# Kernel optimization log

Measured on AMD Instinct MI355X. Metric: run time of the kernel, lower is better.

## Reference

```python
import jax, jax.numpy as jnp
import numpy as np

D = 384      # d_model
DM = 256     # memory feature dim
DF = 1536    # dim_feedforward
EPS = 1e-5


def _layer_norm(x, g, b):
    m = jnp.mean(x, axis=-1, keepdims=True)
    v = jnp.mean(jnp.square(x - m), axis=-1, keepdims=True)
    return (x - m) * jax.lax.rsqrt(v + EPS) * g + b


def setup_inputs() -> dict:
    key = jax.random.key(0)
    ks = jax.random.split(key, 24)
    B, T, T1, Tc = 8, 2048, 2048, 2048
    s = 0.02
    inp = {
        "tgt": jax.random.normal(ks[0], (B, T, D), jnp.float32),
        "memory": jax.random.normal(ks[1], (B, T1, DM), jnp.float32),
        "a1": jnp.float32(0.5),
        "score_c": jax.random.normal(ks[2], (B, 1, Tc, T1), jnp.float32) * 0.1,
        "out_c": jax.random.normal(ks[3], (B, Tc, D), jnp.float32),
        # attention projections
        "Wq": jax.random.normal(ks[4], (D, D), jnp.float32) * s,
        "bq": jnp.zeros((D,), jnp.float32),
        "Wk": jax.random.normal(ks[5], (DM, D), jnp.float32) * s,
        "bk": jnp.zeros((D,), jnp.float32),
        "Wv": jax.random.normal(ks[6], (DM, D), jnp.float32) * s,
        "bv": jnp.zeros((D,), jnp.float32),
        "Wu": jax.random.normal(ks[7], (D, D), jnp.float32) * s,  # unknown
        "bu": jnp.zeros((D,), jnp.float32),
        "Wn": jax.random.normal(ks[8], (D, D), jnp.float32) * s,  # known
        "bn": jnp.zeros((D,), jnp.float32),
        # FFN
        "W1": jax.random.normal(ks[9], (D, DF), jnp.float32) * s,
        "b1": jnp.zeros((DF,), jnp.float32),
        "W2": jax.random.normal(ks[10], (DF, D), jnp.float32) * s,
        "b2": jnp.zeros((D,), jnp.float32),
        # LayerNorms
        "g1": jnp.ones((D,), jnp.float32),
        "be1": jnp.zeros((D,), jnp.float32),
        "g2": jnp.ones((D,), jnp.float32),
        "be2": jnp.zeros((D,), jnp.float32),
    }
    return inp


def reference(tgt, memory, a1, score_c, out_c,
              Wq, bq, Wk, bk, Wv, bv, Wu, bu, Wn, bn,
              W1, b1, W2, b2, g1, be1, g2, be2):
    # --- En_De_Attention (n_head = 1; dropout p=0 / eval mode -> identity) ---
    scale = 1.0 / jnp.sqrt(jnp.float32(D))
    q = tgt @ Wq + bq                  # [B,T,D]
    k = memory @ Wk + bk               # [B,T1,D]
    v = memory @ Wv + bv               # [B,T1,D]
    att = jnp.einsum('btd,bsd->bts', q, k) * scale            # [B,T,T1]

    unknow = tgt @ Wu + bu             # [B,T,D]
    know = out_c @ Wn + bn             # [B,Tc,D]
    score1 = jnp.einsum('btd,bcd->btc', unknow, know) * scale  # [B,T,Tc]
    mixed = jnp.einsum('btc,bcs->bts', score1, score_c[:, 0])  # [B,T,T1]

    # tt = a1 in (0,1]: blended-score branch of the original module
    score = a1 * jax.nn.softmax(mixed, axis=-1) \
          + (1.0 - a1) * jax.nn.softmax(att, axis=-1)          # [B,T,T1]
    z = jnp.einsum('bts,bsd->btd', score, v)                   # [B,T,D]

    # --- residual + norm1 ---
    x = _layer_norm(tgt + z, g1, be1)
    # --- FFN (relu) + residual + norm2 (dropout eval -> identity) ---
    ff = jax.nn.relu(x @ W1 + b1) @ W2 + b2
    out = _layer_norm(x + ff, g2, be2)
    # score2 returned with head dim, matching torch shape [B,1,T,T1]
    return out, score[:, None]
```

## Files before the change

kernel.cpp:

```cpp
#include <hip/hip_runtime.h>
#include <stdint.h>

typedef __attribute__((ext_vector_type(8))) short bf16x8;
typedef __attribute__((ext_vector_type(4))) float f32x4;

__device__ __forceinline__ short f2bf(float f) {
    union { float f; unsigned u; } v; v.f = f;
    unsigned r = v.u + 0x7fffu + ((v.u >> 16) & 1u);
    return (short)(r >> 16);
}
__device__ __forceinline__ float bf2f(short s) {
    union { unsigned u; float f; } v;
    v.u = ((unsigned)(unsigned short)s) << 16;
    return v.f;
}

__device__ __forceinline__ void gld16(const void* g, void* l) {
    auto gp = reinterpret_cast<const __attribute__((address_space(1))) unsigned int*>(
        reinterpret_cast<uintptr_t>(g));
    auto lp = reinterpret_cast<__attribute__((address_space(3))) unsigned int*>(
        reinterpret_cast<uintptr_t>(l));
    __builtin_amdgcn_global_load_lds(gp, lp, 16, 0, 0);
}

template<int OUTBF, int BIASMODE , int DORELU>
__global__ __launch_bounds__(256, 2) void gemmWide(
    const short* __restrict__ Ag, const short* __restrict__ Bg,
    void* __restrict__ Cg, const float* __restrict__ bias,
    int K, int lda, int ldb, int ldc,
    long long sA, long long sB, long long sC,
    long long dA, long long dB, long long dC, float scale)
{
    __shared__ short lds[3 * 12288];
    const int t = threadIdx.x;
    const int lane = t & 63;
    const int wave = t >> 6;
    const int wm = wave >> 1, wn = wave & 1;

    const int gx = gridDim.x, gy = gridDim.y;
    const int nwg = gx * gy * gridDim.z;
    int id = blockIdx.x + gx * (blockIdx.y + gy * blockIdx.z);
    id = (id & 7) * (nwg >> 3) + (id >> 3);
    const int bx = id % gx;
    const int by = (id / gx) % gy;
    const int bz = id / (gx * gy);
    const int zlo = bz & 7, zhi = bz >> 3;

    const long long row0 = (long long)by * 128;
    const long long col0 = (long long)bx * 256;
    const int NT = K >> 5;

    const int gk = ((t & 3) ^ ((t >> 2) & 3) ^ ((t >> 4) & 3)) * 8;
    const short* Asrc = Ag + zlo * sA + zhi * dA + (row0 + (t >> 2)) * (long long)lda + gk;
    const short* Bsrc = Bg + zlo * sB + zhi * dB + (col0 + (t >> 2)) * (long long)ldb + gk;

    const int frow = lane & 15;
    const int fcol = ((lane >> 4) ^ (frow & 3) ^ ((frow >> 2) & 3)) * 8;

    f32x4 acc[4][8] = {};

#define STG(BUF, KC) do { \
        gld16(Asrc + (KC), &lds[(BUF) * 12288 + t * 8]); \
        gld16(Asrc + (KC) + 64LL * lda, &lds[(BUF) * 12288 + 2048 + t * 8]); \
        gld16(Bsrc + (KC), &lds[(BUF) * 12288 + 4096 + t * 8]); \
        gld16(Bsrc + (KC) + 64LL * ldb, &lds[(BUF) * 12288 + 6144 + t * 8]); \
        gld16(Bsrc + (KC) + 128LL * ldb, &lds[(BUF) * 12288 + 8192 + t * 8]); \
        gld16(Bsrc + (KC) + 192LL * ldb, &lds[(BUF) * 12288 + 10240 + t * 8]); } while (0)

    STG(0, 0);
    STG(1, 32);
    asm volatile("s_waitcnt vmcnt(6)\ns_barrier" ::: "memory");

    for (int kt = 0; kt < NT; ++kt) {
        const int rb = (kt % 3) * 12288;
        bf16x8 av[4], bv[8];
#pragma unroll
        for (int m = 0; m < 4; ++m)
            av[m] = *(const bf16x8*)&lds[rb + (wm * 64 + m * 16 + frow) * 32 + fcol];
#pragma unroll
        for (int n = 0; n < 8; ++n)
            bv[n] = *(const bf16x8*)&lds[rb + 4096 + (wn * 128 + n * 16 + frow) * 32 + fcol];
        if (kt + 2 < NT) STG((kt + 2) % 3, (long long)(kt + 2) * 32);
        __builtin_amdgcn_s_setprio(1);
#pragma unroll
        for (int m = 0; m < 4; ++m)
#pragma unroll
            for (int n = 0; n < 8; ++n)
                acc[m][n] = __builtin_amdgcn_mfma_f32_16x16x32_bf16(av[m], bv[n], acc[m][n], 0, 0, 0);
        __builtin_amdgcn_s_setprio(0);
        if (kt + 1 < NT) {
            if (kt + 2 < NT) asm volatile("s_waitcnt vmcnt(6)\ns_barrier" ::: "memory");
            else             asm volatile("s_waitcnt vmcnt(0)\ns_barrier" ::: "memory");
        }
    }
#undef STG

    const int crow = (lane >> 4) * 4;
    const int ccol = lane & 15;
    const long long cz = zlo * sC + zhi * dC;
#pragma unroll
    for (int m = 0; m < 4; ++m)
#pragma unroll
        for (int n = 0; n < 8; ++n)
#pragma unroll
            for (int i = 0; i < 4; ++i) {
                long long r = row0 + wm * 64 + m * 16 + crow + i;
                long long c = col0 + wn * 128 + n * 16 + ccol;
                float v = acc[m][n][i] * scale;
                if (BIASMODE == 1) v += bias[c];
                if (DORELU) v = fmaxf(v, 0.0f);
                long long idx = cz + r * (long long)ldc + c;
                if (OUTBF) ((short*)Cg)[idx] = f2bf(v);
                else ((float*)Cg)[idx] = v;
            }
}

template<int OUTBF, int BIASMODE , int DORELU>
__global__ __launch_bounds__(256, 3) void gemm128r(
    const short* __restrict__ Ag, const short* __restrict__ Bg,
    void* __restrict__ Cg, const float* __restrict__ bias,
    int K, int lda, int ldb, int ldc,
    long long sA, long long sB, long long sC,
    long long dA, long long dB, long long dC, float scale)
{
    __shared__ short lds[3 * 8192];
    const int t = threadIdx.x;
    const int lane = t & 63;
    const int wave = t >> 6;
    const int wm = wave >> 1, wn = wave & 1;

    const int gx = gridDim.x, gy = gridDim.y;
    const int nwg = gx * gy * gridDim.z;
    int id = blockIdx.x + gx * (blockIdx.y + gy * blockIdx.z);
    id = (id & 7) * (nwg >> 3) + (id >> 3);
    const int bx = id % gx;
    const int by = (id / gx) % gy;
    const int bz = id / (gx * gy);
    const int zlo = bz & 7, zhi = bz >> 3;

    const long long row0 = (long long)by * 128;
    const long long col0 = (long long)bx * 128;
    const int NT = K >> 5;

    const int gk = ((t & 3) ^ ((t >> 2) & 3) ^ ((t >> 4) & 3)) * 8;
    const short* Asrc = Ag + zlo * sA + zhi * dA + (row0 + (t >> 2)) * (long long)lda + gk;
    const short* Bsrc = Bg + zlo * sB + zhi * dB + (col0 + (t >> 2)) * (long long)ldb + gk;

    const int frow = lane & 15;
    const int fcol = ((lane >> 4) ^ (frow & 3) ^ ((frow >> 2) & 3)) * 8;

    f32x4 acc[4][4] = {};

#define STG(BUF, KC) do { \
        gld16(Asrc + (KC), &lds[(BUF) * 8192 + t * 8]); \
        gld16(Asrc + (KC) + 64LL * lda, &lds[(BUF) * 8192 + 2048 + t * 8]); \
        gld16(Bsrc + (KC), &lds[(BUF) * 8192 + 4096 + t * 8]); \
        gld16(Bsrc + (KC) + 64LL * ldb, &lds[(BUF) * 8192 + 6144 + t * 8]); } while (0)

    STG(0, 0);
    STG(1, 32);
    asm volatile("s_waitcnt vmcnt(4)\ns_barrier" ::: "memory");

    for (int kt = 0; kt < NT; ++kt) {
        const int rb = (kt % 3) * 8192;
        bf16x8 av[4], bv[4];
#pragma unroll
        for (int m = 0; m < 4; ++m)
            av[m] = *(const bf16x8*)&lds[rb + (wm * 64 + m * 16 + frow) * 32 + fcol];
#pragma unroll
        for (int n = 0; n < 4; ++n)
            bv[n] = *(const bf16x8*)&lds[rb + 4096 + (wn * 64 + n * 16 + frow) * 32 + fcol];
        if (kt + 2 < NT) STG((kt + 2) % 3, (long long)(kt + 2) * 32);
        __builtin_amdgcn_s_setprio(1);
#pragma unroll
        for (int m = 0; m < 4; ++m)
#pragma unroll
            for (int n = 0; n < 4; ++n)
                acc[m][n] = __builtin_amdgcn_mfma_f32_16x16x32_bf16(av[m], bv[n], acc[m][n], 0, 0, 0);
        __builtin_amdgcn_s_setprio(0);
        if (kt + 1 < NT) {
            if (kt + 2 < NT) asm volatile("s_waitcnt vmcnt(4)\ns_barrier" ::: "memory");
            else             asm volatile("s_waitcnt vmcnt(0)\ns_barrier" ::: "memory");
        }
    }
#undef STG

    const int crow = (lane >> 4) * 4;
    const int ccol = lane & 15;
    const long long cz = zlo * sC + zhi * dC;
#pragma unroll
    for (int m = 0; m < 4; ++m)
#pragma unroll
        for (int n = 0; n < 4; ++n)
#pragma unroll
            for (int i = 0; i < 4; ++i) {
                long long r = row0 + wm * 64 + m * 16 + crow + i;
                long long c = col0 + wn * 64 + n * 16 + ccol;
                float v = acc[m][n][i] * scale;
                if (BIASMODE == 1) v += bias[c];
                if (BIASMODE == 2) v += bias[r];
                if (DORELU) v = fmaxf(v, 0.0f);
                long long idx = cz + r * (long long)ldc + c;
                if (OUTBF) ((short*)Cg)[idx] = f2bf(v);
                else ((float*)Cg)[idx] = v;
            }
}

#define RD_A(RB, M, KS) (*(const bf16x8*)&lds[(RB) + (wm * 64 + (M) * 16 + frow) * 64 + \
        ((((KS) << 2) | fq) ^ (frow & 7)) * 8])
#define RD_B(RB, Nn, KS) (*(const bf16x8*)&lds[(RB) + 8192 + (wn * 64 + (Nn) * 16 + frow) * 64 + \
        ((((KS) << 2) | fq) ^ (frow & 7)) * 8])

__global__ __launch_bounds__(256, 2) void gemm128pz(
    const short* __restrict__ A1, const short* __restrict__ B1, short* __restrict__ C1,
    const float* __restrict__ bias1, int K1, int lda1, int ldb1, int ldc1,
    long long sB1, long long sC1,
    const short* __restrict__ A2, const short* __restrict__ B2, short* __restrict__ C2,
    const float* __restrict__ bias2, int K2, int lda2, int ldb2, int ldc2,
    long long sB2, long long sC2)
{
    __shared__ short lds[2 * 16384];
    const int t = threadIdx.x;
    const int lane = t & 63;
    const int wave = t >> 6;
    const int wm = wave >> 1, wn = wave & 1;

    const int gx = gridDim.x, gy = gridDim.y;
    const int nwg = gx * gy * gridDim.z;
    int id = blockIdx.x + gx * (blockIdx.y + gy * blockIdx.z);
    id = (id & 7) * (nwg >> 3) + (id >> 3);
    const int bx = id % gx;
    const int by = (id / gx) % gy;
    const int bz = id / (gx * gy);

    const bool sel = bz >= 8;
    const int zz = bz & 7;
    const short* Ag = sel ? A2 : A1;
    const short* Bg = sel ? B2 : B1;
    short* Cg = sel ? C2 : C1;
    const float* bias = sel ? bias2 : bias1;
    const int K = sel ? K2 : K1;
    const int lda = sel ? lda2 : lda1;
    const int ldb = sel ? ldb2 : ldb1;
    const int ldc = sel ? ldc2 : ldc1;
    const long long sB = sel ? sB2 : sB1;
    const long long sC = sel ? sC2 : sC1;

    const long long row0 = (long long)by * 128;
    const long long col0 = (long long)bx * 128;
    const int NT = K >> 6;

    const int srow = t >> 3;
    const int gk = ((t & 7) ^ (srow & 7)) * 8;
    const short* Asrc = Ag + (row0 + srow) * (long long)lda + gk;
    const short* Bsrc = Bg + (long long)zz * sB + (col0 + srow) * (long long)ldb + gk;

    const int frow = lane & 15;
    const int fq = lane >> 4;

    f32x4 acc[4][4] = {};

#define STAGE_A(WB, KC) do { _Pragma("unroll") \
        for (int r = 0; r < 4; ++r) \
            gld16(Asrc + (KC) + (long long)r * 32 * lda, &lds[(WB) + t * 8 + r * 2048]); } while (0)
#define STAGE_B(WB, KC) do { _Pragma("unroll") \
        for (int r = 0; r < 4; ++r) \
            gld16(Bsrc + (KC) + (long long)r * 32 * ldb, &lds[(WB) + 8192 + t * 8 + r * 2048]); } while (0)

    STAGE_A(0, 0);
    STAGE_B(0, 0);
    asm volatile("s_waitcnt vmcnt(0)\ns_barrier" ::: "memory");

    for (int kt = 0; kt < NT; ++kt) {
        const int rb = (kt & 1) << 14;
        const int wb = ((kt + 1) & 1) << 14;
        const bool st = (kt + 1) < NT;
        const long long kc = (long long)(kt + 1) << 6;

        bf16x8 av[4], bv[4];

#pragma unroll
        for (int m = 0; m < 4; ++m) av[m] = RD_A(rb, m, 0);
#pragma unroll
        for (int n = 0; n < 4; ++n) bv[n] = RD_B(rb, n, 0);
        if (st) STAGE_A(wb, kc);
        asm volatile("s_barrier" ::: "memory");
        __builtin_amdgcn_s_setprio(1);
#pragma unroll
        for (int m = 0; m < 4; ++m)
#pragma unroll
            for (int n = 0; n < 4; ++n)
                acc[m][n] = __builtin_amdgcn_mfma_f32_16x16x32_bf16(av[m], bv[n], acc[m][n], 0, 0, 0);
        __builtin_amdgcn_s_setprio(0);
        asm volatile("s_barrier" ::: "memory");

#pragma unroll
        for (int m = 0; m < 4; ++m) av[m] = RD_A(rb, m, 1);
#pragma unroll
        for (int n = 0; n < 4; ++n) bv[n] = RD_B(rb, n, 1);
        if (st) STAGE_B(wb, kc);
        asm volatile("s_barrier" ::: "memory");
        __builtin_amdgcn_s_setprio(1);
#pragma unroll
        for (int m = 0; m < 4; ++m)
#pragma unroll
            for (int n = 0; n < 4; ++n)
                acc[m][n] = __builtin_amdgcn_mfma_f32_16x16x32_bf16(av[m], bv[n], acc[m][n], 0, 0, 0);
        __builtin_amdgcn_s_setprio(0);
        if (st) asm volatile("s_waitcnt vmcnt(0)\ns_barrier" ::: "memory");
        else    asm volatile("s_barrier" ::: "memory");
    }
#undef STAGE_A
#undef STAGE_B

    const int crow = (lane >> 4) * 4;
    const int ccol = lane & 15;
    const long long cz = (long long)zz * sC;
#pragma unroll
    for (int m = 0; m < 4; ++m)
#pragma unroll
        for (int n = 0; n < 4; ++n)
#pragma unroll
            for (int i = 0; i < 4; ++i) {
                long long r = row0 + wm * 64 + m * 16 + crow + i;
                long long c = col0 + wn * 64 + n * 16 + ccol;
                float v = acc[m][n][i] + bias[r];
                Cg[cz + r * (long long)ldc + c] = f2bf(v);
            }
}
#undef RD_A
#undef RD_B

__global__ __launch_bounds__(256) void cast_all(
    const float* __restrict__ tgt, const float* __restrict__ mem, const float* __restrict__ outc,
    const float* __restrict__ bq, const float* __restrict__ bu,
    short* __restrict__ tgtb, short* __restrict__ memb, short* __restrict__ outcb,
    float* __restrict__ qubias)
{
    const long long R1 = 1572864;
    const long long R2 = R1 + 1048576;
    const long long R3 = R2 + 1572864;
    const long long R4 = R3 + 192;
    long long i = (long long)blockIdx.x * 256 + threadIdx.x;
    const float* in; short* out; long long j;
    if (i < R1) { in = tgt; out = tgtb; j = i; }
    else if (i < R2) { in = mem; out = memb; j = i - R1; }
    else if (i < R3) { in = outc; out = outcb; j = i - R2; }
    else if (i < R4) {
        j = i - R3;
        ((float4*)qubias)[j] = (j < 96) ? ((const float4*)bq)[j] : ((const float4*)bu)[j - 96];
        return;
    } else return;
    float4 v = ((const float4*)in)[j];
    short4 o;
    o.x = f2bf(v.x); o.y = f2bf(v.y); o.z = f2bf(v.z); o.w = f2bf(v.w);
    ((short4*)out)[j] = o;
}

__global__ __launch_bounds__(256) void transpose_all(
    const float* __restrict__ Wq, const float* __restrict__ Wk, const float* __restrict__ Wv,
    const float* __restrict__ Wu, const float* __restrict__ Wn,
    const float* __restrict__ W1, const float* __restrict__ W2,
    short* __restrict__ WquT, short* __restrict__ WkT, short* __restrict__ WvT,
    short* __restrict__ WnT, short* __restrict__ W1T, short* __restrict__ W2T)
{
    __shared__ float tile[64][65];
    int b = blockIdx.x;
    const float* in; short* out; int R, C, local;
    if (b < 36)       { in = Wq; out = WquT;          R = 384;  C = 384;  local = b; }
    else if (b < 60)  { in = Wk; out = WkT;           R = 256;  C = 384;  local = b - 36; }
    else if (b < 84)  { in = Wv; out = WvT;           R = 256;  C = 384;  local = b - 60; }
    else if (b < 120) { in = Wu; out = WquT + 147456; R = 384;  C = 384;  local = b - 84; }
    else if (b < 156) { in = Wn; out = WnT;           R = 384;  C = 384;  local = b - 120; }
    else if (b < 300) { in = W1; out = W1T;           R = 384;  C = 1536; local = b - 156; }
    else              { in = W2; out = W2T;           R = 1536; C = 384;  local = b - 300; }
    const int nbx = C >> 6;
    const int r0 = (local / nbx) * 64, c0 = (local % nbx) * 64;
    const int lr = threadIdx.x >> 6, lc = threadIdx.x & 63;
#pragma unroll
    for (int i = 0; i < 16; ++i) {
        int r = lr * 16 + i;
        tile[r][lc] = in[(long long)(r0 + r) * C + c0 + lc];
    }
    __syncthreads();
#pragma unroll
    for (int i = 0; i < 16; ++i) {
        int r = lr * 16 + i;
        out[(long long)(c0 + r) * R + r0 + lc] = f2bf(tile[lc][r]);
    }
}

__global__ __launch_bounds__(256) void transpose_cast(
    const float* __restrict__ in, short* __restrict__ out,
    int R, int C, long long sIn, long long sOut)
{
    __shared__ float tile[64][65];
    const long long zi = (long long)blockIdx.z * sIn;
    const long long zo = (long long)blockIdx.z * sOut;
    const int r0 = blockIdx.y * 64, c0 = blockIdx.x * 64;
    const int lr = threadIdx.x >> 6, lc = threadIdx.x & 63;
#pragma unroll
    for (int i = 0; i < 16; ++i) {
        int r = lr * 16 + i;
        tile[r][lc] = in[zi + (long long)(r0 + r) * C + c0 + lc];
    }
    __syncthreads();
#pragma unroll
    for (int i = 0; i < 16; ++i) {
        int r = lr * 16 + i;
        out[zo + (long long)(c0 + r) * R + r0 + lc] = f2bf(tile[lc][r]);
    }
}

__global__ __launch_bounds__(256) void softmax_blend(
    const short* __restrict__ attb, const short* __restrict__ mixb,
    const float* __restrict__ a1p,
    float* __restrict__ outF, short* __restrict__ outB)
{
    const int S = 2048;
    const long long row = blockIdx.x;
    const short* ar = attb + row * S;
    const short* mr = mixb + row * S;
    const int t = threadIdx.x;
    const int wave = t >> 6;

    bf16x8 a8 = *(const bf16x8*)&ar[t * 8];
    bf16x8 m8 = *(const bf16x8*)&mr[t * 8];
    float av[8], mv[8];
#pragma unroll
    for (int i = 0; i < 8; ++i) { av[i] = bf2f(a8[i]); mv[i] = bf2f(m8[i]); }

    float amax = av[0], mmax = mv[0];
#pragma unroll
    for (int i = 1; i < 8; ++i) { amax = fmaxf(amax, av[i]); mmax = fmaxf(mmax, mv[i]); }
#pragma unroll
    for (int o = 32; o; o >>= 1) {
        amax = fmaxf(amax, __shfl_xor(amax, o));
        mmax = fmaxf(mmax, __shfl_xor(mmax, o));
    }
    __shared__ float red[2][4];
    if ((t & 63) == 0) { red[0][wave] = amax; red[1][wave] = mmax; }
    __syncthreads();
    amax = fmaxf(fmaxf(red[0][0], red[0][1]), fmaxf(red[0][2], red[0][3]));
    mmax = fmaxf(fmaxf(red[1][0], red[1][1]), fmaxf(red[1][2], red[1][3]));

    float asum = 0.f, msum = 0.f;
#pragma unroll
    for (int i = 0; i < 8; ++i) {
        av[i] = __expf(av[i] - amax); asum += av[i];
        mv[i] = __expf(mv[i] - mmax); msum += mv[i];
    }
#pragma unroll
    for (int o = 32; o; o >>= 1) {
        asum += __shfl_xor(asum, o);
        msum += __shfl_xor(msum, o);
    }
    __shared__ float red2[2][4];
    if ((t & 63) == 0) { red2[0][wave] = asum; red2[1][wave] = msum; }
    __syncthreads();
    asum = red2[0][0] + red2[0][1] + red2[0][2] + red2[0][3];
    msum = red2[1][0] + red2[1][1] + red2[1][2] + red2[1][3];

    const float a1 = a1p[0];
    const float wm = a1 / msum;
    const float wa = (1.0f - a1) / asum;

    float o0[8];
    bf16x8 ob;
#pragma unroll
    for (int i = 0; i < 8; ++i) {
        float s = wm * mv[i] + wa * av[i];
        o0[i] = s;
        ob[i] = f2bf(s);
    }
    float4 f0, f1;
    f0.x = o0[0]; f0.y = o0[1]; f0.z = o0[2]; f0.w = o0[3];
    f1.x = o0[4]; f1.y = o0[5]; f1.z = o0[6]; f1.w = o0[7];
    *(float4*)&outF[row * S + t * 8] = f0;
    *(float4*)&outF[row * S + t * 8 + 4] = f1;
    *(bf16x8*)&outB[row * S + t * 8] = ob;
}

template<int WRITE_BF, int TWO_Y>
__global__ __launch_bounds__(256) void ln_kernel(
    const float* __restrict__ X, const float* __restrict__ Yr,
    const float* __restrict__ Y2,
    const float* __restrict__ g, const float* __restrict__ be,
    float* __restrict__ outF, short* __restrict__ outB)
{
    const int Dm = 384;
    const int wave = threadIdx.x >> 6, lane = threadIdx.x & 63;
    const long long row = (long long)blockIdx.x * 4 + wave;
    const float* x = X + row * Dm;
    const float* y = Yr + row * Dm;
    const float* y2 = TWO_Y ? (Y2 + row * Dm) : nullptr;
    float h[6];
    float s = 0.f, s2 = 0.f;
#pragma unroll
    for (int j = 0; j < 6; ++j) {
        int c = j * 64 + lane;
        h[j] = x[c] + y[c];
        if (TWO_Y) h[j] += y2[c];
        s += h[j]; s2 += h[j] * h[j];
    }
#pragma unroll
    for (int o = 32; o; o >>= 1) { s += __shfl_xor(s, o); s2 += __shfl_xor(s2, o); }
    const float mean = s * (1.0f / 384.0f);
    const float var = s2 * (1.0f / 384.0f) - mean * mean;
    const float rstd = rsqrtf(var + 1e-5f);
#pragma unroll
    for (int j = 0; j < 6; ++j) {
        int c = j * 64 + lane;
        float v = (h[j] - mean) * rstd * g[c] + be[c];
        outF[row * Dm + c] = v;
        if (WRITE_BF) outB[row * Dm + c] = f2bf(v);
    }
}

extern "C" void kernel_launch(void* const* d_in, const int* in_sizes, int n_in,
                              void* d_out, int out_size, void* d_ws, size_t ws_size,
                              hipStream_t stream) {
    const float* tgt     = (const float*)d_in[0];
    const float* memory  = (const float*)d_in[1];
    const float* a1      = (const float*)d_in[2];
    const float* score_c = (const float*)d_in[3];
    const float* out_c   = (const float*)d_in[4];
    const float* Wq = (const float*)d_in[5];  const float* bq = (const float*)d_in[6];
    const float* Wk = (const float*)d_in[7];  const float* bk = (const float*)d_in[8];
    const float* Wv = (const float*)d_in[9];  const float* bv = (const float*)d_in[10];
    const float* Wu = (const float*)d_in[11]; const float* bu = (const float*)d_in[12];
    const float* Wn = (const float*)d_in[13]; const float* bn = (const float*)d_in[14];
    const float* W1 = (const float*)d_in[15]; const float* b1 = (const float*)d_in[16];
    const float* W2 = (const float*)d_in[17]; const float* b2 = (const float*)d_in[18];
    const float* g1 = (const float*)d_in[19]; const float* be1 = (const float*)d_in[20];
    const float* g2 = (const float*)d_in[21]; const float* be2 = (const float*)d_in[22];

    const long long BT = 16384;
    const long long S2 = 2048LL * 2048;
    const long long PB = 2048LL * 384;
    char* ws = (char*)d_ws;
    size_t off = 0;
    auto A_ = [&](size_t b) { size_t r = off; off += (b + 255) & ~(size_t)255; return r; };

    const size_t oTgtB  = A_(BT * 384 * 2);
    const size_t oMemB  = A_(BT * 256 * 2);
    const size_t oOutcB = A_(BT * 384 * 2);
    const size_t oWquT  = A_(768 * 384 * 2);
    const size_t oWnT   = A_(384 * 384 * 2);
    const size_t oWkT   = A_(384 * 256 * 2);
    const size_t oWvT   = A_(384 * 256 * 2);
    const size_t oW1T   = A_(1536 * 384 * 2);
    const size_t oW2T   = A_(384 * 1536 * 2);
    const size_t oQUb   = A_(768 * 4);
    const size_t oQU    = A_(16 * PB * 2);
    const size_t oKP    = A_(16 * PB * 2);
    const size_t oVT    = A_(8LL * 384 * 2048 * 2);
    const size_t oJ     = A_(8 * S2 * 2);
    const size_t oKr    = A_(8 * S2 * 2);
    const size_t oAM    = A_(16 * S2 * 2);
    const size_t oX     = A_(BT * 384 * 4);
    const size_t oXB    = A_(BT * 384 * 2);

    short* tgt_bf  = (short*)(ws + oTgtB);
    short* mem_bf  = (short*)(ws + oMemB);
    short* outc_bf = (short*)(ws + oOutcB);
    short* WquT = (short*)(ws + oWquT);
    short* WnT  = (short*)(ws + oWnT);
    short* WkT  = (short*)(ws + oWkT);
    short* WvT  = (short*)(ws + oWvT);
    short* W1T  = (short*)(ws + oW1T);
    short* W2T  = (short*)(ws + oW2T);
    float* qu_bias = (float*)(ws + oQUb);
    short* qu_bf  = (short*)(ws + oQU);
    short* k_bf   = (short*)(ws + oKP);
    short* Pt_bf  = k_bf + 8 * PB;
    short* vT_bf  = (short*)(ws + oVT);
    short* score_bf = (short*)(ws + oJ);
    short* scoreCt  = (short*)(ws + oKr);
    float* z0_f     = (float*)(ws + oKr);
    float* z1_f     = z0_f + 6291456;
    short* knoT_bf  = (short*)(ws + oAM);
    short* att_bf   = (short*)(ws + oAM);
    short* mix_bf   = att_bf + 8 * S2;
    short* h_bf     = (short*)(ws + oAM);
    float* ff_f     = (float*)(ws + oAM + 8 * S2 * 2);
    float* x_f  = (float*)(ws + oX);
    short* x_bf = (short*)(ws + oXB);

    float* outMain = (float*)d_out;
    float* outScore = (float*)d_out + 6291456;

    const float SC = 0.05103103630798288f;
    dim3 blk(256);

    cast_all<<<16385, blk, 0, stream>>>(tgt, memory, out_c, bq, bu,
                                        tgt_bf, mem_bf, outc_bf, qu_bias);
    transpose_all<<<444, blk, 0, stream>>>(Wq, Wk, Wv, Wu, Wn, W1, W2,
                                           WquT, WkT, WvT, WnT, W1T, W2T);
    transpose_cast<<<dim3(32, 32, 8), blk, 0, stream>>>(score_c, scoreCt, 2048, 2048, S2, S2);

    gemmWide<1, 1, 0><<<dim3(3, 128, 1), blk, 0, stream>>>(
        tgt_bf, WquT, qu_bf, qu_bias, 384, 384, 384, 768, 0, 0, 0, 0, 0, 0, 1.0f);
    gemm128r<1, 1, 0><<<dim3(3, 128, 1), blk, 0, stream>>>(
        mem_bf, WkT, k_bf, bk, 256, 256, 256, 384, 0, 0, 0, 0, 0, 0, 1.0f);
    gemm128pz<<<dim3(16, 3, 16), blk, 0, stream>>>(
        WvT, mem_bf, vT_bf, bv, 256, 256, 256, 2048, 2048LL * 256, PB,
        WnT, outc_bf, knoT_bf, bn, 384, 384, 384, 2048, PB, PB);
    gemm128r<1, 0, 0><<<dim3(3, 16, 8), blk, 0, stream>>>(
        scoreCt, knoT_bf, Pt_bf, nullptr, 2048, 2048, 2048, 384,
        S2, PB, PB, 0, 0, 0, 1.0f);
    gemmWide<1, 0, 0><<<dim3(8, 16, 16), blk, 0, stream>>>(
        qu_bf, k_bf, att_bf, nullptr, 384, 768, 384, 2048,
        2048LL * 768, PB, S2, 384, 8 * PB, 8 * S2, SC);
    softmax_blend<<<16384, blk, 0, stream>>>(att_bf, mix_bf, a1, outScore, score_bf);
    gemm128r<0, 0, 0><<<dim3(3, 16, 16), blk, 0, stream>>>(
        score_bf, vT_bf, z0_f, nullptr, 1024, 2048, 2048, 384,
        S2, PB, PB, 1024, 1024, 6291456, 1.0f);
    ln_kernel<1, 1><<<4096, blk, 0, stream>>>(tgt, z0_f, z1_f, g1, be1, x_f, x_bf);
    gemmWide<1, 1, 1><<<dim3(6, 128, 1), blk, 0, stream>>>(
        x_bf, W1T, h_bf, b1, 384, 384, 384, 1536, 0, 0, 0, 0, 0, 0, 1.0f);
    gemm128r<0, 1, 0><<<dim3(3, 128, 1), blk, 0, stream>>>(
        h_bf, W2T, ff_f, b2, 1536, 1536, 1536, 384, 0, 0, 0, 0, 0, 0, 1.0f);
    ln_kernel<0, 0><<<4096, blk, 0, stream>>>(x_f, ff_f, nullptr, g2, be2, outMain, nullptr);
}
```

Before: 446.9 us.

## Fuse prologue kernels, merge Q/K projections, drop fp32 LN1 output

Combines the cast, weight-transpose and score_c transpose kernels into one launch. Merges the QU and K projection GEMMs into a new 3-stage pipelined kernel with a block-id swizzle. LN1 now writes only bf16, and LN2 reads that bf16 tensor as its residual, which removes an fp32 write and read at some cost in residual precision. The FFN up-projection switches to the gemm128r tile kernel.

Result: faster. 430.4 us (-3.7%).

```diff
diff --git a/kernel.cpp b/kernel.cpp
--- a/kernel.cpp
+++ b/kernel.cpp
@@ -206,6 +206,100 @@
             }
 }
 
+__global__ __launch_bounds__(256, 3) void gemm128rr(
+    const short* __restrict__ A1, const short* __restrict__ B1,
+    short* __restrict__ C1, const float* __restrict__ bias1,
+    int K1, int lda1, int ldb1, int ldc1,
+    const short* __restrict__ A2, const short* __restrict__ B2,
+    short* __restrict__ C2, const float* __restrict__ bias2,
+    int K2, int lda2, int ldb2, int ldc2)
+{
+    __shared__ short lds[3 * 8192];
+    const int t = threadIdx.x;
+    const int lane = t & 63;
+    const int wave = t >> 6;
+    const int wm = wave >> 1, wn = wave & 1;
+
+    const int gx = gridDim.x, gy = gridDim.y;
+    const int nwg = gx * gy;
+    int id = blockIdx.x + gx * blockIdx.y;
+    id = (id & 7) * (nwg >> 3) + (id >> 3);
+    const int bx = id % gx;
+    const int by = id / gx;
+
+    const bool sel = bx >= 6;
+    const int bxx = sel ? bx - 6 : bx;
+    const short* Ag = sel ? A2 : A1;
+    const short* Bg = sel ? B2 : B1;
+    short* Cg = sel ? C2 : C1;
+    const float* bias = sel ? bias2 : bias1;
+    const int K = sel ? K2 : K1;
+    const int lda = sel ? lda2 : lda1;
+    const int ldb = sel ? ldb2 : ldb1;
+    const int ldc = sel ? ldc2 : ldc1;
+
+    const long long row0 = (long long)by * 128;
+    const long long col0 = (long long)bxx * 128;
+    const int NT = K >> 5;
+
+    const int gk = ((t & 3) ^ ((t >> 2) & 3) ^ ((t >> 4) & 3)) * 8;
+    const short* Asrc = Ag + (row0 + (t >> 2)) * (long long)lda + gk;
+    const short* Bsrc = Bg + (col0 + (t >> 2)) * (long long)ldb + gk;
+
+    const int frow = lane & 15;
+    const int fcol = ((lane >> 4) ^ (frow & 3) ^ ((frow >> 2) & 3)) * 8;
+
+    f32x4 acc[4][4] = {};
+
+#define STG(BUF, KC) do { \
+        gld16(Asrc + (KC), &lds[(BUF) * 8192 + t * 8]); \
+        gld16(Asrc + (KC) + 64LL * lda, &lds[(BUF) * 8192 + 2048 + t * 8]); \
+        gld16(Bsrc + (KC), &lds[(BUF) * 8192 + 4096 + t * 8]); \
+        gld16(Bsrc + (KC) + 64LL * ldb, &lds[(BUF) * 8192 + 6144 + t * 8]); } while (0)
+
+    STG(0, 0);
+    STG(1, 32);
+    asm volatile("s_waitcnt vmcnt(4)\ns_barrier" ::: "memory");
+
+    for (int kt = 0; kt < NT; ++kt) {
+        const int rb = (kt % 3) * 8192;
+        bf16x8 av[4], bv[4];
+#pragma unroll
+        for (int m = 0; m < 4; ++m)
+            av[m] = *(const bf16x8*)&lds[rb + (wm * 64 + m * 16 + frow) * 32 + fcol];
+#pragma unroll
+        for (int n = 0; n < 4; ++n)
+            bv[n] = *(const bf16x8*)&lds[rb + 4096 + (wn * 64 + n * 16 + frow) * 32 + fcol];
+        if (kt + 2 < NT) STG((kt + 2) % 3, (long long)(kt + 2) * 32);
+        __builtin_amdgcn_s_setprio(1);
+#pragma unroll
+        for (int m = 0; m < 4; ++m)
+#pragma unroll
+            for (int n = 0; n < 4; ++n)
+                acc[m][n] = __builtin_amdgcn_mfma_f32_16x16x32_bf16(av[m], bv[n], acc[m][n], 0, 0, 0);
+        __builtin_amdgcn_s_setprio(0);
+        if (kt + 1 < NT) {
+            if (kt + 2 < NT) asm volatile("s_waitcnt vmcnt(4)\ns_barrier" ::: "memory");
+            else             asm volatile("s_waitcnt vmcnt(0)\ns_barrier" ::: "memory");
+        }
+    }
+#undef STG
+
+    const int crow = (lane >> 4) * 4;
+    const int ccol = lane & 15;
+#pragma unroll
+    for (int m = 0; m < 4; ++m)
+#pragma unroll
+        for (int n = 0; n < 4; ++n)
+#pragma unroll
+            for (int i = 0; i < 4; ++i) {
+                long long r = row0 + wm * 64 + m * 16 + crow + i;
+                long long c = col0 + wn * 64 + n * 16 + ccol;
+                float v = acc[m][n][i] + bias[c];
+                Cg[r * (long long)ldc + c] = f2bf(v);
+            }
+}
+
 #define RD_A(RB, M, KS) (*(const bf16x8*)&lds[(RB) + (wm * 64 + (M) * 16 + frow) * 64 + \
         ((((KS) << 2) | fq) ^ (frow & 7)) * 8])
 #define RD_B(RB, Nn, KS) (*(const bf16x8*)&lds[(RB) + 8192 + (wn * 64 + (Nn) * 16 + frow) * 64 + \
@@ -331,84 +425,90 @@
 #undef RD_A
 #undef RD_B
 
-__global__ __launch_bounds__(256) void cast_all(
+__global__ __launch_bounds__(256) void prologue(
     const float* __restrict__ tgt, const float* __restrict__ mem, const float* __restrict__ outc,
     const float* __restrict__ bq, const float* __restrict__ bu,
     short* __restrict__ tgtb, short* __restrict__ memb, short* __restrict__ outcb,
-    float* __restrict__ qubias)
-{
-    const long long R1 = 1572864;
-    const long long R2 = R1 + 1048576;
-    const long long R3 = R2 + 1572864;
-    const long long R4 = R3 + 192;
-    long long i = (long long)blockIdx.x * 256 + threadIdx.x;
-    const float* in; short* out; long long j;
-    if (i < R1) { in = tgt; out = tgtb; j = i; }
-    else if (i < R2) { in = mem; out = memb; j = i - R1; }
-    else if (i < R3) { in = outc; out = outcb; j = i - R2; }
-    else if (i < R4) {
-        j = i - R3;
-        ((float4*)qubias)[j] = (j < 96) ? ((const float4*)bq)[j] : ((const float4*)bu)[j - 96];
-        return;
-    } else return;
-    float4 v = ((const float4*)in)[j];
-    short4 o;
-    o.x = f2bf(v.x); o.y = f2bf(v.y); o.z = f2bf(v.z); o.w = f2bf(v.w);
-    ((short4*)out)[j] = o;
-}
-
-__global__ __launch_bounds__(256) void transpose_all(
+    float* __restrict__ qubias,
     const float* __restrict__ Wq, const float* __restrict__ Wk, const float* __restrict__ Wv,
     const float* __restrict__ Wu, const float* __restrict__ Wn,
     const float* __restrict__ W1, const float* __restrict__ W2,
     short* __restrict__ WquT, short* __restrict__ WkT, short* __restrict__ WvT,
-    short* __restrict__ WnT, short* __restrict__ W1T, short* __restrict__ W2T)
+    short* __restrict__ WnT, short* __restrict__ W1T, short* __restrict__ W2T,
+    const float* __restrict__ score_c, short* __restrict__ scoreCt)
 {
     __shared__ float tile[64][65];
-    int b = blockIdx.x;
-    const float* in; short* out; int R, C, local;
-    if (b < 36)       { in = Wq; out = WquT;          R = 384;  C = 384;  local = b; }
-    else if (b < 60)  { in = Wk; out = WkT;           R = 256;  C = 384;  local = b - 36; }
-    else if (b < 84)  { in = Wv; out = WvT;           R = 256;  C = 384;  local = b - 60; }
-    else if (b < 120) { in = Wu; out = WquT + 147456; R = 384;  C = 384;  local = b - 84; }
-    else if (b < 156) { in = Wn; out = WnT;           R = 384;  C = 384;  local = b - 120; }
-    else if (b < 300) { in = W1; out = W1T;           R = 384;  C = 1536; local = b - 156; }
-    else              { in = W2; out = W2T;           R = 1536; C = 384;  local = b - 300; }
-    const int nbx = C >> 6;
-    const int r0 = (local / nbx) * 64, c0 = (local % nbx) * 64;
+    const int blk = blockIdx.x;
+
+    if (blk < 16385) {
+        const long long R1 = 1572864;
+        const long long R2 = R1 + 1048576;
+        const long long R3 = R2 + 1572864;
+        const long long R4 = R3 + 192;
+        long long i = (long long)blk * 256 + threadIdx.x;
+        const float* in; short* out; long long j;
+        if (i < R1) { in = tgt; out = tgtb; j = i; }
+        else if (i < R2) { in = mem; out = memb; j = i - R1; }
+        else if (i < R3) { in = outc; out = outcb; j = i - R2; }
+        else if (i < R4) {
+            j = i - R3;
+            ((float4*)qubias)[j] = (j < 96) ? ((const float4*)bq)[j] : ((const float4*)bu)[j - 96];
+            return;
+        } else return;
+        float4 v = ((const float4*)in)[j];
+        short4 o;
+        o.x = f2bf(v.x); o.y = f2bf(v.y); o.z = f2bf(v.z); o.w = f2bf(v.w);
+        ((short4*)out)[j] = o;
+        return;
+    }
+
     const int lr = threadIdx.x >> 6, lc = threadIdx.x & 63;
-#pragma unroll
-    for (int i = 0; i < 16; ++i) {
-        int r = lr * 16 + i;
-        tile[r][lc] = in[(long long)(r0 + r) * C + c0 + lc];
-    }
-    __syncthreads();
-#pragma unroll
-    for (int i = 0; i < 16; ++i) {
-        int r = lr * 16 + i;
-        out[(long long)(c0 + r) * R + r0 + lc] = f2bf(tile[lc][r]);
-    }
-}
-
-__global__ __launch_bounds__(256) void transpose_cast(
-    const float* __restrict__ in, short* __restrict__ out,
-    int R, int C, long long sIn, long long sOut)
-{
-    __shared__ float tile[64][65];
-    const long long zi = (long long)blockIdx.z * sIn;
-    const long long zo = (long long)blockIdx.z * sOut;
-    const int r0 = blockIdx.y * 64, c0 = blockIdx.x * 64;
-    const int lr = threadIdx.x >> 6, lc = threadIdx.x & 63;
-#pragma unroll
-    for (int i = 0; i < 16; ++i) {
-        int r = lr * 16 + i;
-        tile[r][lc] = in[zi + (long long)(r0 + r) * C + c0 + lc];
-    }
-    __syncthreads();
-#pragma unroll
-    for (int i = 0; i < 16; ++i) {
-        int r = lr * 16 + i;
-        out[zo + (long long)(c0 + r) * R + r0 + lc] = f2bf(tile[lc][r]);
+
+    if (blk < 16829) {
+        int b = blk - 16385;
+        const float* in; short* out; int R, C, local;
+        if (b < 36)       { in = Wq; out = WquT;          R = 384;  C = 384;  local = b; }
+        else if (b < 60)  { in = Wk; out = WkT;           R = 256;  C = 384;  local = b - 36; }
+        else if (b < 84)  { in = Wv; out = WvT;           R = 256;  C = 384;  local = b - 60; }
+        else if (b < 120) { in = Wu; out = WquT + 147456; R = 384;  C = 384;  local = b - 84; }
+        else if (b < 156) { in = Wn; out = WnT;           R = 384;  C = 384;  local = b - 120; }
+        else if (b < 300) { in = W1; out = W1T;           R = 384;  C = 1536; local = b - 156; }
+        else              { in = W2; out = W2T;           R = 1536; C = 384;  local = b - 300; }
+        const int nbx = C >> 6;
+        const int r0 = (local / nbx) * 64, c0 = (local % nbx) * 64;
+#pragma unroll
+        for (int i = 0; i < 16; ++i) {
+            int r = lr * 16 + i;
+            tile[r][lc] = in[(long long)(r0 + r) * C + c0 + lc];
+        }
+        __syncthreads();
+#pragma unroll
+        for (int i = 0; i < 16; ++i) {
+            int r = lr * 16 + i;
+            out[(long long)(c0 + r) * R + r0 + lc] = f2bf(tile[lc][r]);
+        }
+        return;
+    }
+
+    {
+        const long long S2 = 2048LL * 2048;
+        int local = blk - 16829;
+        const int bx = local & 31;
+        const int by = (local >> 5) & 31;
+        const int bz = local >> 10;
+        const long long zi = (long long)bz * S2;
+        const int r0 = by * 64, c0 = bx * 64;
+#pragma unroll
+        for (int i = 0; i < 16; ++i) {
+            int r = lr * 16 + i;
+            tile[r][lc] = score_c[zi + (long long)(r0 + r) * 2048 + c0 + lc];
+        }
+        __syncthreads();
+#pragma unroll
+        for (int i = 0; i < 16; ++i) {
+            int r = lr * 16 + i;
+            scoreCt[zi + (long long)(c0 + r) * 2048 + r0 + lc] = f2bf(tile[lc][r]);
+        }
     }
 }
 
@@ -481,9 +581,9 @@
     *(bf16x8*)&outB[row * S + t * 8] = ob;
 }
 
-template<int WRITE_BF, int TWO_Y>
+template<int WRITE_F, int WRITE_BF, int TWO_Y, int XBF>
 __global__ __launch_bounds__(256) void ln_kernel(
-    const float* __restrict__ X, const float* __restrict__ Yr,
+    const void* __restrict__ Xv, const float* __restrict__ Yr,
     const float* __restrict__ Y2,
     const float* __restrict__ g, const float* __restrict__ be,
     float* __restrict__ outF, short* __restrict__ outB)
@@ -491,7 +591,6 @@
     const int Dm = 384;
     const int wave = threadIdx.x >> 6, lane = threadIdx.x & 63;
     const long long row = (long long)blockIdx.x * 4 + wave;
-    const float* x = X + row * Dm;
     const float* y = Yr + row * Dm;
     const float* y2 = TWO_Y ? (Y2 + row * Dm) : nullptr;
     float h[6];
@@ -499,7 +598,10 @@
 #pragma unroll
     for (int j = 0; j < 6; ++j) {
         int c = j * 64 + lane;
-        h[j] = x[c] + y[c];
+        float xv;
+        if (XBF) xv = bf2f(((const short*)Xv)[row * Dm + c]);
+        else     xv = ((const float*)Xv)[row * Dm + c];
+        h[j] = xv + y[c];
         if (TWO_Y) h[j] += y2[c];
         s += h[j]; s2 += h[j] * h[j];
     }
@@ -512,7 +614,7 @@
     for (int j = 0; j < 6; ++j) {
         int c = j * 64 + lane;
         float v = (h[j] - mean) * rstd * g[c] + be[c];
-        outF[row * Dm + c] = v;
+        if (WRITE_F) outF[row * Dm + c] = v;
         if (WRITE_BF) outB[row * Dm + c] = f2bf(v);
     }
 }
@@ -558,7 +660,6 @@
     const size_t oJ     = A_(8 * S2 * 2);
     const size_t oKr    = A_(8 * S2 * 2);
     const size_t oAM    = A_(16 * S2 * 2);
-    const size_t oX     = A_(BT * 384 * 4);
     const size_t oXB    = A_(BT * 384 * 2);
 
     short* tgt_bf  = (short*)(ws + oTgtB);
@@ -584,7 +685,6 @@
     short* mix_bf   = att_bf + 8 * S2;
     short* h_bf     = (short*)(ws + oAM);
     float* ff_f     = (float*)(ws + oAM + 8 * S2 * 2);
-    float* x_f  = (float*)(ws + oX);
     short* x_bf = (short*)(ws + oXB);
 
     float* outMain = (float*)d_out;
@@ -593,16 +693,14 @@
     const float SC = 0.05103103630798288f;
     dim3 blk(256);
 
-    cast_all<<<16385, blk, 0, stream>>>(tgt, memory, out_c, bq, bu,
-                                        tgt_bf, mem_bf, outc_bf, qu_bias);
-    transpose_all<<<444, blk, 0, stream>>>(Wq, Wk, Wv, Wu, Wn, W1, W2,
-                                           WquT, WkT, WvT, WnT, W1T, W2T);
-    transpose_cast<<<dim3(32, 32, 8), blk, 0, stream>>>(score_c, scoreCt, 2048, 2048, S2, S2);
-
-    gemmWide<1, 1, 0><<<dim3(3, 128, 1), blk, 0, stream>>>(
-        tgt_bf, WquT, qu_bf, qu_bias, 384, 384, 384, 768, 0, 0, 0, 0, 0, 0, 1.0f);
-    gemm128r<1, 1, 0><<<dim3(3, 128, 1), blk, 0, stream>>>(
-        mem_bf, WkT, k_bf, bk, 256, 256, 256, 384, 0, 0, 0, 0, 0, 0, 1.0f);
+    prologue<<<25021, blk, 0, stream>>>(
+        tgt, memory, out_c, bq, bu, tgt_bf, mem_bf, outc_bf, qu_bias,
+        Wq, Wk, Wv, Wu, Wn, W1, W2, WquT, WkT, WvT, WnT, W1T, W2T,
+        score_c, scoreCt);
+
+    gemm128rr<<<dim3(9, 128, 1), blk, 0, stream>>>(
+        tgt_bf, WquT, qu_bf, qu_bias, 384, 384, 384, 768,
+        mem_bf, WkT, k_bf, bk, 256, 256, 256, 384);
     gemm128pz<<<dim3(16, 3, 16), blk, 0, stream>>>(
         WvT, mem_bf, vT_bf, bv, 256, 256, 256, 2048, 2048LL * 256, PB,
         WnT, outc_bf, knoT_bf, bn, 384, 384, 384, 2048, PB, PB);
@@ -616,10 +714,12 @@
     gemm128r<0, 0, 0><<<dim3(3, 16, 16), blk, 0, stream>>>(
         score_bf, vT_bf, z0_f, nullptr, 1024, 2048, 2048, 384,
         S2, PB, PB, 1024, 1024, 6291456, 1.0f);
-    ln_kernel<1, 1><<<4096, blk, 0, stream>>>(tgt, z0_f, z1_f, g1, be1, x_f, x_bf);
-    gemmWide<1, 1, 1><<<dim3(6, 128, 1), blk, 0, stream>>>(
+    ln_kernel<0, 1, 1, 0><<<4096, blk, 0, stream>>>(
+        tgt, z0_f, z1_f, g1, be1, nullptr, x_bf);
+    gemm128r<1, 1, 1><<<dim3(12, 128, 1), blk, 0, stream>>>(
         x_bf, W1T, h_bf, b1, 384, 384, 384, 1536, 0, 0, 0, 0, 0, 0, 1.0f);
     gemm128r<0, 1, 0><<<dim3(3, 128, 1), blk, 0, stream>>>(
         h_bf, W2T, ff_f, b2, 1536, 1536, 1536, 384, 0, 0, 0, 0, 0, 0, 1.0f);
-    ln_kernel<0, 0><<<4096, blk, 0, stream>>>(x_f, ff_f, nullptr, g2, be2, outMain, nullptr);
-}
+    ln_kernel<1, 0, 0, 1><<<4096, blk, 0, stream>>>(
+        x_bf, ff_f, nullptr, g2, be2, outMain, nullptr);
+}
```
